# Performance work log

Measured on AMD Instinct MI355X. Metric: run time of the kernel, lower is better.

Reference implementation:

```python
import jax, jax.numpy as jnp
import numpy as np

B, C, S, HEADS, MLP = 8, 128, 32, 8, 512
EPS = 1e-5
SCALE = (C // HEADS) ** -0.5  # dim_head=16 -> 16**-0.5


def setup_inputs() -> dict:
    key = jax.random.key(0)
    ks = jax.random.split(key, 6)
    x = jax.random.normal(ks[0], (B, C, S, S, S), jnp.float32)
    qkv_w = jax.random.normal(ks[1], (3 * C, C), jnp.float32) * 0.02   # Conv3d 1x1x1, no bias
    proj_w = jax.random.normal(ks[2], (C, C), jnp.float32) * 0.02
    proj_b = jnp.zeros((C,), jnp.float32)
    ln1_w = jnp.ones((C, S, S, S), jnp.float32)
    ln1_b = jnp.zeros((C, S, S, S), jnp.float32)
    ln2_w = jnp.ones((C, S, S, S), jnp.float32)
    ln2_b = jnp.zeros((C, S, S, S), jnp.float32)
    mlp_w1 = jax.random.normal(ks[3], (MLP, C), jnp.float32) * 0.02
    mlp_b1 = jnp.zeros((MLP,), jnp.float32)
    mlp_w2 = jax.random.normal(ks[4], (C, MLP), jnp.float32) * 0.02
    mlp_b2 = jnp.zeros((C,), jnp.float32)
    return dict(x=x, qkv_w=qkv_w, proj_w=proj_w, proj_b=proj_b,
                ln1_w=ln1_w, ln1_b=ln1_b, ln2_w=ln2_w, ln2_b=ln2_b,
                mlp_w1=mlp_w1, mlp_b1=mlp_b1, mlp_w2=mlp_w2, mlp_b2=mlp_b2)


def _layernorm_full(x, w, b):
    # LayerNorm over (channel, D, H, W) per batch element, biased variance, eps=1e-5
    mu = jnp.mean(x, axis=(1, 2, 3, 4), keepdims=True)
    var = jnp.mean(jnp.square(x - mu), axis=(1, 2, 3, 4), keepdims=True)
    return (x - mu) * jax.lax.rsqrt(var + EPS) * w[None] + b[None]


def _block(x, qkv_w, proj_w, proj_b, ln1_w, ln1_b, ln2_w, ln2_b,
           mlp_w1, mlp_b1, mlp_w2, mlp_b2):
    b, c, d, h, w = x.shape
    n = d * h * w
    ch = c // HEADS
    xf = x.reshape(b, c, n)
    # 1x1x1 conv == per-voxel matmul over channels
    qkv = jnp.einsum('bcn,oc->bon', xf, qkv_w)                 # [b, 3c, n]
    q, k, v = jnp.split(qkv, 3, axis=1)
    q = q.reshape(b, HEADS, ch, n)
    k = k.reshape(b, HEADS, ch, n)
    v = v.reshape(b, HEADS, ch, n)
    # channel-channel attention: contraction over spatial tokens n
    attn = jax.nn.softmax(jnp.einsum('bhin,bhjn->bhij', q, k) * SCALE, axis=-1)
    out = jnp.einsum('bhij,bhjn->bhin', attn, v).reshape(b, c, n)
    out = jnp.einsum('bcn,oc->bon', out, proj_w) + proj_b[None, :, None]
    x1 = _layernorm_full(x + out.reshape(b, c, d, h, w), ln1_w, ln1_b)
    # MLP: conv1x1 -> exact GELU -> conv1x1
    x1f = x1.reshape(b, c, n)
    hid = jax.nn.gelu(jnp.einsum('bcn,oc->bon', x1f, mlp_w1) + mlp_b1[None, :, None],
                      approximate=False)
    m = jnp.einsum('bon,co->bcn', hid, mlp_w2) + mlp_b2[None, :, None]
    return _layernorm_full(x1 + m.reshape(b, c, d, h, w), ln2_w, ln2_b)


def reference(x, qkv_w, proj_w, proj_b, ln1_w, ln1_b, ln2_w, ln2_b,
              mlp_w1, mlp_b1, mlp_w2, mlp_b2):
    return _block(x, qkv_w, proj_w, proj_b, ln1_w, ln1_b, ln2_w, ln2_b,
                  mlp_w1, mlp_b1, mlp_w2, mlp_b2)
```

## Files before the change

kernel.cpp:

```cpp
#include <hip/hip_runtime.h>
#include <hip/hip_bf16.h>
#include <math.h>


#define N_SP 32768
typedef __hip_bfloat16 bf16;
static const size_t DS = (size_t)128 * N_SP;

typedef __attribute__((ext_vector_type(8))) short s8b;
typedef __attribute__((ext_vector_type(4))) float f4;

__device__ __forceinline__ ushort f2b(float f) {
    __hip_bfloat16 h = __float2bfloat16(f);
    return *reinterpret_cast<ushort*>(&h);
}
__device__ __forceinline__ float b2f(ushort u) {
    unsigned v = ((unsigned)u) << 16;
    float f;
    __builtin_memcpy(&f, &v, 4);
    return f;
}
__device__ __forceinline__ float gelu_f(float h) {
    float u = 1.5957691216057308f * h * fmaf(0.044715f, h * h, 1.0f);
    float e = __expf(u);
    return h * (1.0f - __builtin_amdgcn_rcpf(e + 1.0f));
}
__device__ __forceinline__ int swz8(int n, int c0) {
    return n * 128 + (c0 ^ ((n & 15) << 3));
}
__device__ __forceinline__ int swz4(int n, int c0) {
    return n * 128 + (((c0 & 0x78) ^ ((n & 15) << 3)) | (c0 & 4));
}

__global__ __launch_bounds__(256) void k_transpose(const float* __restrict__ in,
                                                   float* __restrict__ out,
                                                   int R, int Ccols) {
    int idx = blockIdx.x * 256 + threadIdx.x;
    if (idx >= R * Ccols) return;
    int r = idx / Ccols, c = idx % Ccols;
    out[c * R + r] = in[idx];
}

__global__ __launch_bounds__(256) void k_cvt(const float* __restrict__ in,
                                             ushort* __restrict__ out, int n) {
    int i = blockIdx.x * 256 + threadIdx.x;
    if (i < n) out[i] = f2b(in[i]);
}

__global__ __launch_bounds__(256) void k_packln(const float* __restrict__ w,
                                                const float* __restrict__ b,
                                                uint* __restrict__ out) {
    int tid = blockIdx.x * 256 + threadIdx.x;
    int c = tid >> 15, n = tid & 32767;
    uint lo = f2b(w[tid]);
    uint hi = f2b(b[tid]);
    out[(size_t)n * 128 + c] = lo | (hi << 16);
}

__global__ __launch_bounds__(256) void k_packflat(const float* __restrict__ w,
                                                  const float* __restrict__ b,
                                                  uint* __restrict__ out) {
    int tid = blockIdx.x * 256 + threadIdx.x;
    uint lo = f2b(w[tid]);
    uint hi = f2b(b[tid]);
    out[tid] = lo | (hi << 16);
}

__global__ __launch_bounds__(256, 4) void k_cov(const float* __restrict__ x,
                                                float* __restrict__ Gpart) {
    __shared__ ushort xs[128 * 136];
    const int kb = blockIdx.x, b = blockIdx.y;
    const int t = threadIdx.x;
    const int wave = t >> 6, lane = t & 63, q = lane >> 4, r = lane & 15;
    f4 acc[8][2];
#pragma unroll
    for (int m = 0; m < 8; ++m) { acc[m][0] = (f4){0,0,0,0}; acc[m][1] = (f4){0,0,0,0}; }
    for (int ch = 0; ch < 2; ++ch) {
        const int nbase = kb * 256 + ch * 128;
        __syncthreads();
        {
            const int nq = t & 31, cr = t >> 5;
            const float* xp = x + (size_t)b * DS + nbase + nq * 4;
            for (int cc = 0; cc < 16; ++cc) {
                int c = cr * 16 + cc;
                float4 xv = *(const float4*)(xp + (size_t)c * N_SP);
                ushort4 pk;
                pk.x = f2b(xv.x); pk.y = f2b(xv.y);
                pk.z = f2b(xv.z); pk.w = f2b(xv.w);
                *(ushort4*)&xs[c * 136 + nq * 4] = pk;
            }
        }
        __syncthreads();
        for (int kk = 0; kk < 4; ++kk) {
            const int c0 = kk * 32 + q * 8;
            s8b bj0 = *(const s8b*)&xs[(wave * 32 + r) * 136 + c0];
            s8b bj1 = *(const s8b*)&xs[(wave * 32 + 16 + r) * 136 + c0];
#pragma unroll
            for (int m = 0; m < 8; ++m) {
                s8b a = *(const s8b*)&xs[(m * 16 + r) * 136 + c0];
                acc[m][0] = __builtin_amdgcn_mfma_f32_16x16x32_bf16(a, bj0, acc[m][0], 0, 0, 0);
                acc[m][1] = __builtin_amdgcn_mfma_f32_16x16x32_bf16(a, bj1, acc[m][1], 0, 0, 0);
            }
        }
    }
    float* gp = Gpart + ((size_t)b * 128 + kb) * 16384;
#pragma unroll
    for (int n2 = 0; n2 < 2; ++n2)
#pragma unroll
        for (int m = 0; m < 8; ++m)
#pragma unroll
            for (int rg = 0; rg < 4; ++rg) {
                int i = m * 16 + q * 4 + rg;
                int j = wave * 32 + n2 * 16 + r;
                gp[i * 128 + j] = acc[m][n2][rg];
            }
}

__global__ __launch_bounds__(256) void k_greduce(const float* __restrict__ Gpart,
                                                 float* __restrict__ G) {
    int tid = blockIdx.x * 256 + threadIdx.x;
    int b = tid >> 14, ij = tid & 16383;
    float s = 0.f;
    for (int kb = 0; kb < 128; ++kb)
        s += Gpart[((size_t)b * 128 + kb) * 16384 + ij];
    G[tid] = s;
}

__global__ __launch_bounds__(256) void k_gram_small(const float* __restrict__ G,
                                                    const float* __restrict__ qkv_w,
                                                    float* __restrict__ attn) {
    __shared__ float t1[16 * 132];
    __shared__ float sg[16 * 16];
    const int bh = blockIdx.x;
    const int b = bh >> 3, h = bh & 7;
    const int t = threadIdx.x;
    {
        const int i = t >> 4, c20 = (t & 15) * 8;
        const float* wq = qkv_w + (size_t)(h * 16 + i) * 128;
        const float* Gb = G + (size_t)b * 16384;
        float a[8];
#pragma unroll
        for (int k = 0; k < 8; ++k) a[k] = 0.f;
        for (int c = 0; c < 128; ++c) {
            float w = wq[c];
            const float* grow = Gb + c * 128 + c20;
#pragma unroll
            for (int k = 0; k < 8; ++k) a[k] = fmaf(w, grow[k], a[k]);
        }
#pragma unroll
        for (int k = 0; k < 8; ++k) t1[i * 132 + c20 + k] = a[k];
    }
    __syncthreads();
    {
        const int i = t >> 4, j = t & 15;
        const float* wk = qkv_w + (size_t)(128 + h * 16 + j) * 128;
        float s = 0.f;
        for (int c2 = 0; c2 < 128; ++c2) s = fmaf(t1[i * 132 + c2], wk[c2], s);
        sg[i * 16 + j] = s * 0.25f;
    }
    __syncthreads();
    if (t < 16) {
        float mx = -1e30f;
#pragma unroll
        for (int j = 0; j < 16; ++j) mx = fmaxf(mx, sg[t * 16 + j]);
        float e[16], sum = 0.f;
#pragma unroll
        for (int j = 0; j < 16; ++j) { e[j] = expf(sg[t * 16 + j] - mx); sum += e[j]; }
        float inv = 1.0f / sum;
#pragma unroll
        for (int j = 0; j < 16; ++j)
            attn[((size_t)bh * 16 + t) * 16 + j] = e[j] * inv;
    }
}

__global__ __launch_bounds__(256, 2) void k_mfold(const float* __restrict__ attn,
                                                  const float* __restrict__ qkv_w,
                                                  const float* __restrict__ PT,
                                                  ushort* __restrict__ Mbb) {
    __shared__ float t2[128 * 128];
    const int b = blockIdx.x, t = threadIdx.x;
    {
        const int hi = t >> 1, c0 = (t & 1) * 64;
        const int h = hi >> 4;
        const float* at = attn + ((size_t)b * 128 + hi) * 16;
        float a[16];
#pragma unroll
        for (int j = 0; j < 16; ++j) a[j] = at[j];
        float sc[64];
#pragma unroll
        for (int c = 0; c < 64; ++c) sc[c] = 0.f;
        for (int j = 0; j < 16; ++j) {
            const float* wv = qkv_w + (size_t)(256 + h * 16 + j) * 128 + c0;
            float aj = a[j];
#pragma unroll
            for (int c = 0; c < 64; ++c) sc[c] = fmaf(aj, wv[c], sc[c]);
        }
#pragma unroll
        for (int c = 0; c < 64; ++c) t2[hi * 128 + c0 + c] = sc[c];
    }
    __syncthreads();
    const int c = t & 127, half = t >> 7;
    float acc[128];
#pragma unroll
    for (int o = 0; o < 128; ++o) acc[o] = 0.f;
    for (int ci = half * 64; ci < half * 64 + 64; ++ci) {
        float s = t2[ci * 128 + c];
        const float* pt = PT + ci * 128;
#pragma unroll
        for (int o = 0; o < 128; ++o) acc[o] = fmaf(pt[o], s, acc[o]);
    }
    __syncthreads();
    if (half) {
#pragma unroll
        for (int o = 0; o < 128; ++o) t2[c * 128 + o] = acc[o];
    }
    __syncthreads();
    if (!half) {
        ushort* m = Mbb + (size_t)b * 16384;
#pragma unroll
        for (int o = 0; o < 128; ++o)
            m[(size_t)o * 128 + c] = f2b(acc[o] + t2[c * 128 + o]);
    }
}

__global__ __launch_bounds__(256, 3) void k_attnproj(const float* __restrict__ x,
                                                     const ushort* __restrict__ Mbb,
                                                     const float* __restrict__ proj_b,
                                                     float* __restrict__ x1T,
                                                     float* __restrict__ st) {
    __shared__ ushort xT[128 * 136];
    const int b = blockIdx.y;
    const int n0 = blockIdx.x * 128;
    const int t = threadIdx.x;
    const int wave = t >> 6, lane = t & 63, q = lane >> 4, r = lane & 15;
    {
        const int nn = t & 127, cg = t >> 7;
        const float* xp = x + (size_t)b * DS + n0 + nn;
        for (int g = 0; g < 16; ++g) {
            int c0 = cg * 64 + g * 4;
            ushort4 pk;
            pk.x = f2b(xp[(size_t)(c0 + 0) * N_SP]);
            pk.y = f2b(xp[(size_t)(c0 + 1) * N_SP]);
            pk.z = f2b(xp[(size_t)(c0 + 2) * N_SP]);
            pk.w = f2b(xp[(size_t)(c0 + 3) * N_SP]);
            *(ushort4*)&xT[nn * 136 + c0] = pk;
        }
    }
    const int orow = wave * 32 + r;
    s8b a[8];
    {
        const ushort* mp = Mbb + (size_t)b * 16384 + (size_t)orow * 128 + q * 8;
#pragma unroll
        for (int m = 0; m < 2; ++m)
#pragma unroll
            for (int kk = 0; kk < 4; ++kk)
                a[m * 4 + kk] = *(const s8b*)(mp + m * 16 * 128 + kk * 32);
    }
    __syncthreads();
    f4 acc[2][8];
#pragma unroll
    for (int m = 0; m < 2; ++m)
#pragma unroll
        for (int j = 0; j < 8; ++j) acc[m][j] = (f4){0,0,0,0};
#pragma unroll
    for (int kk = 0; kk < 4; ++kk) {
        const int c0 = kk * 32 + q * 8;
#pragma unroll
        for (int j = 0; j < 8; ++j) {
            s8b bx = *(const s8b*)&xT[(j * 16 + r) * 136 + c0];
            acc[0][j] = __builtin_amdgcn_mfma_f32_16x16x32_bf16(a[kk],     bx, acc[0][j], 0, 0, 0);
            acc[1][j] = __builtin_amdgcn_mfma_f32_16x16x32_bf16(a[4 + kk], bx, acc[1][j], 0, 0, 0);
        }
    }
    float s = 0.f, sq = 0.f;
    float4 pbq0 = *(const float4*)&proj_b[wave * 32 + q * 4];
    float4 pbq1 = *(const float4*)&proj_b[wave * 32 + 16 + q * 4];
#pragma unroll
    for (int m = 0; m < 2; ++m) {
        const int o0 = wave * 32 + m * 16 + q * 4;
        const float4 pb = m ? pbq1 : pbq0;
#pragma unroll
        for (int j = 0; j < 8; ++j) {
            const int nn = j * 16 + r;
            ushort4 xr = *(const ushort4*)&xT[nn * 136 + o0];
            float v0 = acc[m][j][0] + pb.x + b2f(xr.x);
            float v1 = acc[m][j][1] + pb.y + b2f(xr.y);
            float v2 = acc[m][j][2] + pb.z + b2f(xr.z);
            float v3 = acc[m][j][3] + pb.w + b2f(xr.w);
            float4 ov; ov.x = v0; ov.y = v1; ov.z = v2; ov.w = v3;
            *(float4*)(x1T + (size_t)b * DS + (size_t)(n0 + nn) * 128 + o0) = ov;
            s += (v0 + v1) + (v2 + v3);
            sq = fmaf(v0, v0, sq); sq = fmaf(v1, v1, sq);
            sq = fmaf(v2, v2, sq); sq = fmaf(v3, v3, sq);
        }
    }
#pragma unroll
    for (int off = 32; off > 0; off >>= 1) {
        s += __shfl_down(s, off, 64);
        sq += __shfl_down(sq, off, 64);
    }
    if (lane == 0) {
        atomicAdd(&st[0 + b], s);
        atomicAdd(&st[8 + b], sq);
    }
}

__global__ void k_finalize(float* st, int off) {
    int b = threadIdx.x;
    if (b < 8) {
        const float invn = 1.0f / 4194304.0f;
        float mu = st[off + b] * invn;
        float var = st[off + 8 + b] * invn - mu * mu;
        st[off + 16 + b] = mu;
        st[off + 24 + b] = rsqrtf(var + 1e-5f);
    }
}

__global__ __launch_bounds__(256) void k_lnapply(const float* __restrict__ in,
                                                 const uint* __restrict__ lnwb,
                                                 const float* __restrict__ st, int off,
                                                 float* __restrict__ out) {
    size_t i4 = (size_t)blockIdx.x * 256 + threadIdx.x;
    int b = (int)(i4 >> 20);
    size_t cn = i4 * 4 - (size_t)b * 4194304;
    float mu = st[off + 16 + b], rs = st[off + 24 + b];
    const float4 xv = *(const float4*)(in + (size_t)b * DS + cn);
    const uint4 wv = *(const uint4*)(lnwb + cn);
    float4 o;
    o.x = fmaf((xv.x - mu) * rs, b2f((ushort)(wv.x & 0xffffu)), b2f((ushort)(wv.x >> 16)));
    o.y = fmaf((xv.y - mu) * rs, b2f((ushort)(wv.y & 0xffffu)), b2f((ushort)(wv.y >> 16)));
    o.z = fmaf((xv.z - mu) * rs, b2f((ushort)(wv.z & 0xffffu)), b2f((ushort)(wv.z >> 16)));
    o.w = fmaf((xv.w - mu) * rs, b2f((ushort)(wv.w & 0xffffu)), b2f((ushort)(wv.w >> 16)));
    *(float4*)(out + (size_t)b * DS + cn) = o;
}

__global__ __launch_bounds__(256, 2) void k_mlp(const float* __restrict__ x1T,
                                                float* __restrict__ xout,
                                                const ushort* __restrict__ w1b,
                                                const float* __restrict__ b1v,
                                                const ushort* __restrict__ w2b,
                                                const float* __restrict__ b2v,
                                                const uint* __restrict__ lnwbT,
                                                float* __restrict__ st) {
    __shared__ ushort xT[128 * 128];
    __shared__ ushort hT[128 * 128];
    const int b = blockIdx.y;
    const int n0 = blockIdx.x * 128;
    const int t = threadIdx.x;
    const int wave = t >> 6, lane = t & 63, q = lane >> 4, r = lane & 15;
    const float mu = st[16 + b], rs = st[24 + b];
    {
        const int cq = (t & 31) * 4;
        const int rb = t >> 5;
        for (int g = 0; g < 16; ++g) {
            int nn = g * 8 + rb;
            float4 xv = *(const float4*)(x1T + (size_t)b * DS + (size_t)(n0 + nn) * 128 + cq);
            uint4  wv = *(const uint4*)(lnwbT + (size_t)(n0 + nn) * 128 + cq);
            ushort4 pk;
            pk.x = f2b(fmaf((xv.x - mu) * rs, b2f((ushort)(wv.x & 0xffffu)), b2f((ushort)(wv.x >> 16))));
            pk.y = f2b(fmaf((xv.y - mu) * rs, b2f((ushort)(wv.y & 0xffffu)), b2f((ushort)(wv.y >> 16))));
            pk.z = f2b(fmaf((xv.z - mu) * rs, b2f((ushort)(wv.z & 0xffffu)), b2f((ushort)(wv.z >> 16))));
            pk.w = f2b(fmaf((xv.w - mu) * rs, b2f((ushort)(wv.w & 0xffffu)), b2f((ushort)(wv.w >> 16))));
            *(ushort4*)&xT[swz4(nn, cq)] = pk;
        }
    }
    const int orow = wave * 32 + r;
    s8b a1[8];
    {
        const ushort* w1p = w1b + (size_t)orow * 128 + q * 8;
#pragma unroll
        for (int m = 0; m < 2; ++m)
#pragma unroll
            for (int kk = 0; kk < 4; ++kk)
                a1[m * 4 + kk] = *(const s8b*)(w1p + m * 16 * 128 + kk * 32);
    }
    __syncthreads();
    f4 acc2[2][8];
#pragma unroll
    for (int m = 0; m < 2; ++m)
#pragma unroll
        for (int j = 0; j < 8; ++j) acc2[m][j] = (f4){0,0,0,0};

    for (int os = 0; os < 4; ++os) {
        f4 acc1[2][8];
#pragma unroll
        for (int m = 0; m < 2; ++m)
#pragma unroll
            for (int j = 0; j < 8; ++j) acc1[m][j] = (f4){0,0,0,0};
#pragma unroll
        for (int kk = 0; kk < 4; ++kk) {
            const int c0 = kk * 32 + q * 8;
#pragma unroll
            for (int j = 0; j < 8; ++j) {
                s8b bx = *(const s8b*)&xT[swz8(j * 16 + r, c0)];
                acc1[0][j] = __builtin_amdgcn_mfma_f32_16x16x32_bf16(a1[kk],     bx, acc1[0][j], 0, 0, 0);
                acc1[1][j] = __builtin_amdgcn_mfma_f32_16x16x32_bf16(a1[4 + kk], bx, acc1[1][j], 0, 0, 0);
            }
        }
        s8b a2[8];
        {
            const ushort* w2p = w2b + (size_t)orow * 512 + os * 128 + q * 8;
#pragma unroll
            for (int m = 0; m < 2; ++m)
#pragma unroll
                for (int kk = 0; kk < 4; ++kk)
                    a2[m * 4 + kk] = *(const s8b*)(w2p + m * 16 * 512 + kk * 32);
        }
        float4 b1q0 = *(const float4*)&b1v[os * 128 + wave * 32 + q * 4];
        float4 b1q1 = *(const float4*)&b1v[os * 128 + wave * 32 + 16 + q * 4];
#pragma unroll
        for (int m = 0; m < 2; ++m) {
            const int hr0 = wave * 32 + m * 16 + q * 4;
            const float4 bq = m ? b1q1 : b1q0;
#pragma unroll
            for (int j = 0; j < 8; ++j) {
                ushort4 pk;
                pk.x = f2b(gelu_f(acc1[m][j][0] + bq.x));
                pk.y = f2b(gelu_f(acc1[m][j][1] + bq.y));
                pk.z = f2b(gelu_f(acc1[m][j][2] + bq.z));
                pk.w = f2b(gelu_f(acc1[m][j][3] + bq.w));
                *(ushort4*)&hT[swz4(j * 16 + r, hr0)] = pk;
            }
        }
        __syncthreads();
#pragma unroll
        for (int kk = 0; kk < 4; ++kk) {
            const int c0 = kk * 32 + q * 8;
#pragma unroll
            for (int j = 0; j < 8; ++j) {
                s8b hx = *(const s8b*)&hT[swz8(j * 16 + r, c0)];
                acc2[0][j] = __builtin_amdgcn_mfma_f32_16x16x32_bf16(a2[kk],     hx, acc2[0][j], 0, 0, 0);
                acc2[1][j] = __builtin_amdgcn_mfma_f32_16x16x32_bf16(a2[4 + kk], hx, acc2[1][j], 0, 0, 0);
            }
        }
        if (os < 3) {
            const ushort* w1p = w1b + (size_t)((os + 1) * 128 + orow) * 128 + q * 8;
#pragma unroll
            for (int m = 0; m < 2; ++m)
#pragma unroll
                for (int kk = 0; kk < 4; ++kk)
                    a1[m * 4 + kk] = *(const s8b*)(w1p + m * 16 * 128 + kk * 32);
        }
        __syncthreads();
    }
    float s = 0.f, sq = 0.f;
    float4 b2q0 = *(const float4*)&b2v[wave * 32 + q * 4];
    float4 b2q1 = *(const float4*)&b2v[wave * 32 + 16 + q * 4];
#pragma unroll
    for (int m = 0; m < 2; ++m) {
        const int o0 = wave * 32 + m * 16 + q * 4;
        const float4 bq = m ? b2q1 : b2q0;
#pragma unroll
        for (int j = 0; j < 8; ++j) {
            const int nn = j * 16 + r;
            ushort4 xr = *(const ushort4*)&xT[swz4(nn, o0)];
            float v0 = acc2[m][j][0] + bq.x + b2f(xr.x);
            float v1 = acc2[m][j][1] + bq.y + b2f(xr.y);
            float v2 = acc2[m][j][2] + bq.z + b2f(xr.z);
            float v3 = acc2[m][j][3] + bq.w + b2f(xr.w);
            float* op = xout + (size_t)b * DS + n0 + nn;
            op[(size_t)(o0 + 0) * N_SP] = v0;
            op[(size_t)(o0 + 1) * N_SP] = v1;
            op[(size_t)(o0 + 2) * N_SP] = v2;
            op[(size_t)(o0 + 3) * N_SP] = v3;
            s += (v0 + v1) + (v2 + v3);
            sq = fmaf(v0, v0, sq); sq = fmaf(v1, v1, sq);
            sq = fmaf(v2, v2, sq); sq = fmaf(v3, v3, sq);
        }
    }
#pragma unroll
    for (int off = 32; off > 0; off >>= 1) {
        s += __shfl_down(s, off, 64);
        sq += __shfl_down(sq, off, 64);
    }
    if (lane == 0) {
        atomicAdd(&st[32 + b], s);
        atomicAdd(&st[40 + b], sq);
    }
}

extern "C" void kernel_launch(void* const* d_in, const int* in_sizes, int n_in,
                              void* d_out, int out_size, void* d_ws, size_t ws_size,
                              hipStream_t stream) {
    const float* x      = (const float*)d_in[0];
    const float* qkv_w  = (const float*)d_in[1];
    const float* proj_w = (const float*)d_in[2];
    const float* proj_b = (const float*)d_in[3];
    const float* ln1_w  = (const float*)d_in[4];
    const float* ln1_b  = (const float*)d_in[5];
    const float* ln2_w  = (const float*)d_in[6];
    const float* ln2_b  = (const float*)d_in[7];
    const float* mlp_w1 = (const float*)d_in[8];
    const float* mlp_b1 = (const float*)d_in[9];
    const float* mlp_w2 = (const float*)d_in[10];
    const float* mlp_b2 = (const float*)d_in[11];
    float* out = (float*)d_out;

    char* wsb = (char*)d_ws;
    float*  st    = (float*)wsb;
    float*  attn  = (float*)(wsb + 256);
    float*  PT    = (float*)(wsb + 65792);
    ushort* Mbb   = (ushort*)(wsb + 131328);
    ushort* w1b   = (ushort*)(wsb + 393472);
    ushort* w2b   = (ushort*)(wsb + 524544);
    float*  G     = (float*)(wsb + 655616);
    uint*   lnwbT = (uint*)(wsb + 1179904);
    float*  Gpart = (float*)(wsb + 18874368);
    float*  x1T   = (float*)(wsb + 18874368);
    uint*   lnwb2 = (uint*)(wsb + 18874368);

    hipMemsetAsync(st, 0, 64 * sizeof(float), stream);

    k_transpose<<<64, 256, 0, stream>>>(proj_w, PT, 128, 128);
    k_cvt<<<256, 256, 0, stream>>>(mlp_w1, w1b, 65536);
    k_cvt<<<256, 256, 0, stream>>>(mlp_w2, w2b, 65536);
    k_packln<<<16384, 256, 0, stream>>>(ln1_w, ln1_b, lnwbT);

    k_cov<<<dim3(128, 8), 256, 0, stream>>>(x, Gpart);
    k_greduce<<<512, 256, 0, stream>>>(Gpart, G);
    k_gram_small<<<64, 256, 0, stream>>>(G, qkv_w, attn);
    k_mfold<<<8, 256, 0, stream>>>(attn, qkv_w, PT, Mbb);

    k_attnproj<<<dim3(256, 8), 256, 0, stream>>>(x, Mbb, proj_b, x1T, st);
    k_finalize<<<1, 64, 0, stream>>>(st, 0);
    k_mlp<<<dim3(256, 8), 256, 0, stream>>>(x1T, out, w1b, mlp_b1, w2b, mlp_b2,
                                            lnwbT, st);
    k_packflat<<<16384, 256, 0, stream>>>(ln2_w, ln2_b, lnwb2);
    k_finalize<<<1, 64, 0, stream>>>(st, 32);
    k_lnapply<<<32768, 256, 0, stream>>>(out, lnwb2, st, 32, out);
}
```

Measured before the change: 974.2 us.

## Halve spatial tiles in attnproj and MLP kernels and batch global loads

```diff
diff --git a/kernel.cpp b/kernel.cpp
--- a/kernel.cpp
+++ b/kernel.cpp
@@ -81,13 +81,20 @@
         {
             const int nq = t & 31, cr = t >> 5;
             const float* xp = x + (size_t)b * DS + nbase + nq * 4;
-            for (int cc = 0; cc < 16; ++cc) {
-                int c = cr * 16 + cc;
-                float4 xv = *(const float4*)(xp + (size_t)c * N_SP);
-                ushort4 pk;
-                pk.x = f2b(xv.x); pk.y = f2b(xv.y);
-                pk.z = f2b(xv.z); pk.w = f2b(xv.w);
-                *(ushort4*)&xs[c * 136 + nq * 4] = pk;
+#pragma unroll
+            for (int half = 0; half < 2; ++half) {
+                float4 xv[8];
+#pragma unroll
+                for (int cc = 0; cc < 8; ++cc)
+                    xv[cc] = *(const float4*)(xp + (size_t)(cr * 16 + half * 8 + cc) * N_SP);
+#pragma unroll
+                for (int cc = 0; cc < 8; ++cc) {
+                    int c = cr * 16 + half * 8 + cc;
+                    ushort4 pk;
+                    pk.x = f2b(xv[cc].x); pk.y = f2b(xv[cc].y);
+                    pk.z = f2b(xv[cc].z); pk.w = f2b(xv[cc].w);
+                    *(ushort4*)&xs[c * 136 + nq * 4] = pk;
+                }
             }
         }
         __syncthreads();
@@ -121,6 +128,7 @@
     int tid = blockIdx.x * 256 + threadIdx.x;
     int b = tid >> 14, ij = tid & 16383;
     float s = 0.f;
+#pragma unroll 8
     for (int kb = 0; kb < 128; ++kb)
         s += Gpart[((size_t)b * 128 + kb) * 16384 + ij];
     G[tid] = s;
@@ -223,27 +231,31 @@
     }
 }
 
-__global__ __launch_bounds__(256, 3) void k_attnproj(const float* __restrict__ x,
+__global__ __launch_bounds__(256, 4) void k_attnproj(const float* __restrict__ x,
                                                      const ushort* __restrict__ Mbb,
                                                      const float* __restrict__ proj_b,
                                                      float* __restrict__ x1T,
                                                      float* __restrict__ st) {
-    __shared__ ushort xT[128 * 136];
+    __shared__ ushort xT[64 * 136];
     const int b = blockIdx.y;
-    const int n0 = blockIdx.x * 128;
+    const int n0 = blockIdx.x * 64;
     const int t = threadIdx.x;
     const int wave = t >> 6, lane = t & 63, q = lane >> 4, r = lane & 15;
     {
-        const int nn = t & 127, cg = t >> 7;
-        const float* xp = x + (size_t)b * DS + n0 + nn;
-        for (int g = 0; g < 16; ++g) {
-            int c0 = cg * 64 + g * 4;
-            ushort4 pk;
-            pk.x = f2b(xp[(size_t)(c0 + 0) * N_SP]);
-            pk.y = f2b(xp[(size_t)(c0 + 1) * N_SP]);
-            pk.z = f2b(xp[(size_t)(c0 + 2) * N_SP]);
-            pk.w = f2b(xp[(size_t)(c0 + 3) * N_SP]);
-            *(ushort4*)&xT[nn * 136 + c0] = pk;
+        const int nq = (t & 15) * 4;
+        const int cr = t >> 4;
+        const float* xb = x + (size_t)b * DS + n0 + nq;
+        float4 xv[8];
+#pragma unroll
+        for (int g = 0; g < 8; ++g)
+            xv[g] = *(const float4*)(xb + (size_t)(cr + g * 16) * N_SP);
+#pragma unroll
+        for (int g = 0; g < 8; ++g) {
+            int c = cr + g * 16;
+            xT[(nq + 0) * 136 + c] = f2b(xv[g].x);
+            xT[(nq + 1) * 136 + c] = f2b(xv[g].y);
+            xT[(nq + 2) * 136 + c] = f2b(xv[g].z);
+            xT[(nq + 3) * 136 + c] = f2b(xv[g].w);
         }
     }
     const int orow = wave * 32 + r;
@@ -257,16 +269,16 @@
                 a[m * 4 + kk] = *(const s8b*)(mp + m * 16 * 128 + kk * 32);
     }
     __syncthreads();
-    f4 acc[2][8];
+    f4 acc[2][4];
 #pragma unroll
     for (int m = 0; m < 2; ++m)
 #pragma unroll
-        for (int j = 0; j < 8; ++j) acc[m][j] = (f4){0,0,0,0};
+        for (int j = 0; j < 4; ++j) acc[m][j] = (f4){0,0,0,0};
 #pragma unroll
     for (int kk = 0; kk < 4; ++kk) {
         const int c0 = kk * 32 + q * 8;
 #pragma unroll
-        for (int j = 0; j < 8; ++j) {
+        for (int j = 0; j < 4; ++j) {
             s8b bx = *(const s8b*)&xT[(j * 16 + r) * 136 + c0];
             acc[0][j] = __builtin_amdgcn_mfma_f32_16x16x32_bf16(a[kk],     bx, acc[0][j], 0, 0, 0);
             acc[1][j] = __builtin_amdgcn_mfma_f32_16x16x32_bf16(a[4 + kk], bx, acc[1][j], 0, 0, 0);
@@ -280,7 +292,7 @@
         const int o0 = wave * 32 + m * 16 + q * 4;
         const float4 pb = m ? pbq1 : pbq0;
 #pragma unroll
-        for (int j = 0; j < 8; ++j) {
+        for (int j = 0; j < 4; ++j) {
             const int nn = j * 16 + r;
             ushort4 xr = *(const ushort4*)&xT[nn * 136 + o0];
             float v0 = acc[m][j][0] + pb.x + b2f(xr.x);
@@ -334,7 +346,7 @@
     *(float4*)(out + (size_t)b * DS + cn) = o;
 }
 
-__global__ __launch_bounds__(256, 2) void k_mlp(const float* __restrict__ x1T,
+__global__ __launch_bounds__(256, 4) void k_mlp(const float* __restrict__ x1T,
                                                 float* __restrict__ xout,
                                                 const ushort* __restrict__ w1b,
                                                 const float* __restrict__ b1v,
@@ -342,26 +354,37 @@
                                                 const float* __restrict__ b2v,
                                                 const uint* __restrict__ lnwbT,
                                                 float* __restrict__ st) {
-    __shared__ ushort xT[128 * 128];
-    __shared__ ushort hT[128 * 128];
+    __shared__ ushort xT[64 * 128];
+    __shared__ ushort hT[64 * 128];
     const int b = blockIdx.y;
-    const int n0 = blockIdx.x * 128;
+    const int n0 = blockIdx.x * 64;
     const int t = threadIdx.x;
     const int wave = t >> 6, lane = t & 63, q = lane >> 4, r = lane & 15;
     const float mu = st[16 + b], rs = st[24 + b];
     {
         const int cq = (t & 31) * 4;
         const int rb = t >> 5;
-        for (int g = 0; g < 16; ++g) {
-            int nn = g * 8 + rb;
-            float4 xv = *(const float4*)(x1T + (size_t)b * DS + (size_t)(n0 + nn) * 128 + cq);
-            uint4  wv = *(const uint4*)(lnwbT + (size_t)(n0 + nn) * 128 + cq);
-            ushort4 pk;
-            pk.x = f2b(fmaf((xv.x - mu) * rs, b2f((ushort)(wv.x & 0xffffu)), b2f((ushort)(wv.x >> 16))));
-            pk.y = f2b(fmaf((xv.y - mu) * rs, b2f((ushort)(wv.y & 0xffffu)), b2f((ushort)(wv.y >> 16))));
-            pk.z = f2b(fmaf((xv.z - mu) * rs, b2f((ushort)(wv.z & 0xffffu)), b2f((ushort)(wv.z >> 16))));
-            pk.w = f2b(fmaf((xv.w - mu) * rs, b2f((ushort)(wv.w & 0xffffu)), b2f((ushort)(wv.w >> 16))));
-            *(ushort4*)&xT[swz4(nn, cq)] = pk;
+        const float* xb = x1T + (size_t)b * DS + (size_t)n0 * 128;
+        const uint*  wb = lnwbT + (size_t)n0 * 128;
+#pragma unroll
+        for (int gb = 0; gb < 2; ++gb) {
+            float4 xv[4]; uint4 wv[4];
+#pragma unroll
+            for (int u = 0; u < 4; ++u) {
+                int nn = (gb * 4 + u) * 8 + rb;
+                xv[u] = *(const float4*)(xb + (size_t)nn * 128 + cq);
+                wv[u] = *(const uint4*)(wb + (size_t)nn * 128 + cq);
+            }
+#pragma unroll
+            for (int u = 0; u < 4; ++u) {
+                int nn = (gb * 4 + u) * 8 + rb;
+                ushort4 pk;
+                pk.x = f2b(fmaf((xv[u].x - mu) * rs, b2f((ushort)(wv[u].x & 0xffffu)), b2f((ushort)(wv[u].x >> 16))));
+                pk.y = f2b(fmaf((xv[u].y - mu) * rs, b2f((ushort)(wv[u].y & 0xffffu)), b2f((ushort)(wv[u].y >> 16))));
+                pk.z = f2b(fmaf((xv[u].z - mu) * rs, b2f((ushort)(wv[u].z & 0xffffu)), b2f((ushort)(wv[u].z >> 16))));
+                pk.w = f2b(fmaf((xv[u].w - mu) * rs, b2f((ushort)(wv[u].w & 0xffffu)), b2f((ushort)(wv[u].w >> 16))));
+                *(ushort4*)&xT[swz4(nn, cq)] = pk;
+            }
         }
     }
     const int orow = wave * 32 + r;
@@ -375,23 +398,23 @@
                 a1[m * 4 + kk] = *(const s8b*)(w1p + m * 16 * 128 + kk * 32);
     }
     __syncthreads();
-    f4 acc2[2][8];
+    f4 acc2[2][4];
 #pragma unroll
     for (int m = 0; m < 2; ++m)
 #pragma unroll
-        for (int j = 0; j < 8; ++j) acc2[m][j] = (f4){0,0,0,0};
+        for (int j = 0; j < 4; ++j) acc2[m][j] = (f4){0,0,0,0};
 
     for (int os = 0; os < 4; ++os) {
-        f4 acc1[2][8];
+        f4 acc1[2][4];
 #pragma unroll
         for (int m = 0; m < 2; ++m)
 #pragma unroll
-            for (int j = 0; j < 8; ++j) acc1[m][j] = (f4){0,0,0,0};
+            for (int j = 0; j < 4; ++j) acc1[m][j] = (f4){0,0,0,0};
 #pragma unroll
         for (int kk = 0; kk < 4; ++kk) {
             const int c0 = kk * 32 + q * 8;
 #pragma unroll
-            for (int j = 0; j < 8; ++j) {
+            for (int j = 0; j < 4; ++j) {
                 s8b bx = *(const s8b*)&xT[swz8(j * 16 + r, c0)];
                 acc1[0][j] = __builtin_amdgcn_mfma_f32_16x16x32_bf16(a1[kk],     bx, acc1[0][j], 0, 0, 0);
                 acc1[1][j] = __builtin_amdgcn_mfma_f32_16x16x32_bf16(a1[4 + kk], bx, acc1[1][j], 0, 0, 0);
@@ -413,7 +436,7 @@
             const int hr0 = wave * 32 + m * 16 + q * 4;
             const float4 bq = m ? b1q1 : b1q0;
 #pragma unroll
-            for (int j = 0; j < 8; ++j) {
+            for (int j = 0; j < 4; ++j) {
                 ushort4 pk;
                 pk.x = f2b(gelu_f(acc1[m][j][0] + bq.x));
                 pk.y = f2b(gelu_f(acc1[m][j][1] + bq.y));
@@ -427,7 +450,7 @@
         for (int kk = 0; kk < 4; ++kk) {
             const int c0 = kk * 32 + q * 8;
 #pragma unroll
-            for (int j = 0; j < 8; ++j) {
+            for (int j = 0; j < 4; ++j) {
                 s8b hx = *(const s8b*)&hT[swz8(j * 16 + r, c0)];
                 acc2[0][j] = __builtin_amdgcn_mfma_f32_16x16x32_bf16(a2[kk],     hx, acc2[0][j], 0, 0, 0);
                 acc2[1][j] = __builtin_amdgcn_mfma_f32_16x16x32_bf16(a2[4 + kk], hx, acc2[1][j], 0, 0, 0);
@@ -451,7 +474,7 @@
         const int o0 = wave * 32 + m * 16 + q * 4;
         const float4 bq = m ? b2q1 : b2q0;
 #pragma unroll
-        for (int j = 0; j < 8; ++j) {
+        for (int j = 0; j < 4; ++j) {
             const int nn = j * 16 + r;
             ushort4 xr = *(const ushort4*)&xT[swz4(nn, o0)];
             float v0 = acc2[m][j][0] + bq.x + b2f(xr.x);
@@ -521,9 +544,9 @@
     k_gram_small<<<64, 256, 0, stream>>>(G, qkv_w, attn);
     k_mfold<<<8, 256, 0, stream>>>(attn, qkv_w, PT, Mbb);
 
-    k_attnproj<<<dim3(256, 8), 256, 0, stream>>>(x, Mbb, proj_b, x1T, st);
+    k_attnproj<<<dim3(512, 8), 256, 0, stream>>>(x, Mbb, proj_b, x1T, st);
     k_finalize<<<1, 64, 0, stream>>>(st, 0);
-    k_mlp<<<dim3(256, 8), 256, 0, stream>>>(x1T, out, w1b, mlp_b1, w2b, mlp_b2,
+    k_mlp<<<dim3(512, 8), 256, 0, stream>>>(x1T, out, w1b, mlp_b1, w2b, mlp_b2,
                                             lnwbT, st);
     k_packflat<<<16384, 256, 0, stream>>>(ln2_w, ln2_b, lnwb2);
     k_finalize<<<1, 64, 0, stream>>>(st, 32);
```

Measured after the change: 1.388 ms. 1.42x slower.

## Store attention-residual intermediate in bf16 and batch global loads for latency hiding

Applied to the files above, without the earlier changes.

```diff
diff --git a/kernel.cpp b/kernel.cpp
--- a/kernel.cpp
+++ b/kernel.cpp
@@ -81,13 +81,20 @@
         {
             const int nq = t & 31, cr = t >> 5;
             const float* xp = x + (size_t)b * DS + nbase + nq * 4;
-            for (int cc = 0; cc < 16; ++cc) {
-                int c = cr * 16 + cc;
-                float4 xv = *(const float4*)(xp + (size_t)c * N_SP);
-                ushort4 pk;
-                pk.x = f2b(xv.x); pk.y = f2b(xv.y);
-                pk.z = f2b(xv.z); pk.w = f2b(xv.w);
-                *(ushort4*)&xs[c * 136 + nq * 4] = pk;
+#pragma unroll
+            for (int half = 0; half < 2; ++half) {
+                float4 xv[8];
+#pragma unroll
+                for (int cc = 0; cc < 8; ++cc)
+                    xv[cc] = *(const float4*)(xp + (size_t)(cr * 16 + half * 8 + cc) * N_SP);
+#pragma unroll
+                for (int cc = 0; cc < 8; ++cc) {
+                    int c = cr * 16 + half * 8 + cc;
+                    ushort4 pk;
+                    pk.x = f2b(xv[cc].x); pk.y = f2b(xv[cc].y);
+                    pk.z = f2b(xv[cc].z); pk.w = f2b(xv[cc].w);
+                    *(ushort4*)&xs[c * 136 + nq * 4] = pk;
+                }
             }
         }
         __syncthreads();
@@ -121,6 +128,7 @@
     int tid = blockIdx.x * 256 + threadIdx.x;
     int b = tid >> 14, ij = tid & 16383;
     float s = 0.f;
+#pragma unroll 8
     for (int kb = 0; kb < 128; ++kb)
         s += Gpart[((size_t)b * 128 + kb) * 16384 + ij];
     G[tid] = s;
@@ -226,7 +234,7 @@
 __global__ __launch_bounds__(256, 3) void k_attnproj(const float* __restrict__ x,
                                                      const ushort* __restrict__ Mbb,
                                                      const float* __restrict__ proj_b,
-                                                     float* __restrict__ x1T,
+                                                     ushort* __restrict__ x1Tb,
                                                      float* __restrict__ st) {
     __shared__ ushort xT[128 * 136];
     const int b = blockIdx.y;
@@ -236,14 +244,19 @@
     {
         const int nn = t & 127, cg = t >> 7;
         const float* xp = x + (size_t)b * DS + n0 + nn;
-        for (int g = 0; g < 16; ++g) {
-            int c0 = cg * 64 + g * 4;
-            ushort4 pk;
-            pk.x = f2b(xp[(size_t)(c0 + 0) * N_SP]);
-            pk.y = f2b(xp[(size_t)(c0 + 1) * N_SP]);
-            pk.z = f2b(xp[(size_t)(c0 + 2) * N_SP]);
-            pk.w = f2b(xp[(size_t)(c0 + 3) * N_SP]);
-            *(ushort4*)&xT[nn * 136 + c0] = pk;
+        for (int gb = 0; gb < 4; ++gb) {
+            float xv[16];
+#pragma unroll
+            for (int u = 0; u < 16; ++u)
+                xv[u] = xp[(size_t)(cg * 64 + gb * 16 + u) * N_SP];
+#pragma unroll
+            for (int u4 = 0; u4 < 4; ++u4) {
+                int c0 = cg * 64 + gb * 16 + u4 * 4;
+                ushort4 pk;
+                pk.x = f2b(xv[u4 * 4 + 0]); pk.y = f2b(xv[u4 * 4 + 1]);
+                pk.z = f2b(xv[u4 * 4 + 2]); pk.w = f2b(xv[u4 * 4 + 3]);
+                *(ushort4*)&xT[nn * 136 + c0] = pk;
+            }
         }
     }
     const int orow = wave * 32 + r;
@@ -287,8 +300,9 @@
             float v1 = acc[m][j][1] + pb.y + b2f(xr.y);
             float v2 = acc[m][j][2] + pb.z + b2f(xr.z);
             float v3 = acc[m][j][3] + pb.w + b2f(xr.w);
-            float4 ov; ov.x = v0; ov.y = v1; ov.z = v2; ov.w = v3;
-            *(float4*)(x1T + (size_t)b * DS + (size_t)(n0 + nn) * 128 + o0) = ov;
+            ushort4 ov;
+            ov.x = f2b(v0); ov.y = f2b(v1); ov.z = f2b(v2); ov.w = f2b(v3);
+            *(ushort4*)(x1Tb + (size_t)b * DS + (size_t)(n0 + nn) * 128 + o0) = ov;
             s += (v0 + v1) + (v2 + v3);
             sq = fmaf(v0, v0, sq); sq = fmaf(v1, v1, sq);
             sq = fmaf(v2, v2, sq); sq = fmaf(v3, v3, sq);
@@ -334,7 +348,7 @@
     *(float4*)(out + (size_t)b * DS + cn) = o;
 }
 
-__global__ __launch_bounds__(256, 2) void k_mlp(const float* __restrict__ x1T,
+__global__ __launch_bounds__(256, 2) void k_mlp(const ushort* __restrict__ x1Tb,
                                                 float* __restrict__ xout,
                                                 const ushort* __restrict__ w1b,
                                                 const float* __restrict__ b1v,
@@ -350,18 +364,43 @@
     const int wave = t >> 6, lane = t & 63, q = lane >> 4, r = lane & 15;
     const float mu = st[16 + b], rs = st[24 + b];
     {
-        const int cq = (t & 31) * 4;
-        const int rb = t >> 5;
-        for (int g = 0; g < 16; ++g) {
-            int nn = g * 8 + rb;
-            float4 xv = *(const float4*)(x1T + (size_t)b * DS + (size_t)(n0 + nn) * 128 + cq);
-            uint4  wv = *(const uint4*)(lnwbT + (size_t)(n0 + nn) * 128 + cq);
-            ushort4 pk;
-            pk.x = f2b(fmaf((xv.x - mu) * rs, b2f((ushort)(wv.x & 0xffffu)), b2f((ushort)(wv.x >> 16))));
-            pk.y = f2b(fmaf((xv.y - mu) * rs, b2f((ushort)(wv.y & 0xffffu)), b2f((ushort)(wv.y >> 16))));
-            pk.z = f2b(fmaf((xv.z - mu) * rs, b2f((ushort)(wv.z & 0xffffu)), b2f((ushort)(wv.z >> 16))));
-            pk.w = f2b(fmaf((xv.w - mu) * rs, b2f((ushort)(wv.w & 0xffffu)), b2f((ushort)(wv.w >> 16))));
-            *(ushort4*)&xT[swz4(nn, cq)] = pk;
+        const int c8 = (t & 15) * 8, rb = t >> 4;
+        const ushort* xb = x1Tb + (size_t)b * DS + (size_t)n0 * 128;
+        const uint*  wb = lnwbT + (size_t)n0 * 128;
+#pragma unroll
+        for (int gb = 0; gb < 2; ++gb) {
+            s8b xv[4]; uint4 wv0[4], wv1[4];
+#pragma unroll
+            for (int u = 0; u < 4; ++u) {
+                int nn = (gb * 4 + u) * 16 + rb;
+                xv[u]  = *(const s8b*)(xb + (size_t)nn * 128 + c8);
+                wv0[u] = *(const uint4*)(wb + (size_t)nn * 128 + c8);
+                wv1[u] = *(const uint4*)(wb + (size_t)nn * 128 + c8 + 4);
+            }
+#pragma unroll
+            for (int u = 0; u < 4; ++u) {
+                int nn = (gb * 4 + u) * 16 + rb;
+                ushort4 p0, p1;
+                float xe;
+                xe = b2f((ushort)xv[u][0]);
+                p0.x = f2b(fmaf((xe - mu) * rs, b2f((ushort)(wv0[u].x & 0xffffu)), b2f((ushort)(wv0[u].x >> 16))));
+                xe = b2f((ushort)xv[u][1]);
+                p0.y = f2b(fmaf((xe - mu) * rs, b2f((ushort)(wv0[u].y & 0xffffu)), b2f((ushort)(wv0[u].y >> 16))));
+                xe = b2f((ushort)xv[u][2]);
+                p0.z = f2b(fmaf((xe - mu) * rs, b2f((ushort)(wv0[u].z & 0xffffu)), b2f((ushort)(wv0[u].z >> 16))));
+                xe = b2f((ushort)xv[u][3]);
+                p0.w = f2b(fmaf((xe - mu) * rs, b2f((ushort)(wv0[u].w & 0xffffu)), b2f((ushort)(wv0[u].w >> 16))));
+                xe = b2f((ushort)xv[u][4]);
+                p1.x = f2b(fmaf((xe - mu) * rs, b2f((ushort)(wv1[u].x & 0xffffu)), b2f((ushort)(wv1[u].x >> 16))));
+                xe = b2f((ushort)xv[u][5]);
+                p1.y = f2b(fmaf((xe - mu) * rs, b2f((ushort)(wv1[u].y & 0xffffu)), b2f((ushort)(wv1[u].y >> 16))));
+                xe = b2f((ushort)xv[u][6]);
+                p1.z = f2b(fmaf((xe - mu) * rs, b2f((ushort)(wv1[u].z & 0xffffu)), b2f((ushort)(wv1[u].z >> 16))));
+                xe = b2f((ushort)xv[u][7]);
+                p1.w = f2b(fmaf((xe - mu) * rs, b2f((ushort)(wv1[u].w & 0xffffu)), b2f((ushort)(wv1[u].w >> 16))));
+                *(ushort4*)&xT[swz4(nn, c8)] = p0;
+                *(ushort4*)&xT[swz4(nn, c8 + 4)] = p1;
+            }
         }
     }
     const int orow = wave * 32 + r;
@@ -506,7 +545,7 @@
     float*  G     = (float*)(wsb + 655616);
     uint*   lnwbT = (uint*)(wsb + 1179904);
     float*  Gpart = (float*)(wsb + 18874368);
-    float*  x1T   = (float*)(wsb + 18874368);
+    ushort* x1Tb  = (ushort*)(wsb + 18874368);
     uint*   lnwb2 = (uint*)(wsb + 18874368);
 
     hipMemsetAsync(st, 0, 64 * sizeof(float), stream);
@@ -521,9 +560,9 @@
     k_gram_small<<<64, 256, 0, stream>>>(G, qkv_w, attn);
     k_mfold<<<8, 256, 0, stream>>>(attn, qkv_w, PT, Mbb);
 
-    k_attnproj<<<dim3(256, 8), 256, 0, stream>>>(x, Mbb, proj_b, x1T, st);
+    k_attnproj<<<dim3(256, 8), 256, 0, stream>>>(x, Mbb, proj_b, x1Tb, st);
     k_finalize<<<1, 64, 0, stream>>>(st, 0);
-    k_mlp<<<dim3(256, 8), 256, 0, stream>>>(x1T, out, w1b, mlp_b1, w2b, mlp_b2,
+    k_mlp<<<dim3(256, 8), 256, 0, stream>>>(x1Tb, out, w1b, mlp_b1, w2b, mlp_b2,
                                             lnwbT, st);
     k_packflat<<<16384, 256, 0, stream>>>(ln2_w, ln2_b, lnwb2);
     k_finalize<<<1, 64, 0, stream>>>(st, 32);
```

After: 970.6 us. No clear change (-0.4%).
